# Performance work log

Measured on AMD Instinct MI355X. Metric: run time of the kernel, lower is better.

Reference implementation:

```python
import jax, jax.numpy as jnp
import numpy as np


def _gelu(x):
    # torch nn.GELU default is the exact (erf) variant
    return jax.nn.gelu(x, approximate=False)


def setup_inputs() -> dict:
    key = jax.random.key(0)
    ks = jax.random.split(key, 10)
    B, IN, H, D, C, K = 32768, 64, 256, 16, 8, 64
    HS = D // 2  # structure_filter hidden (latent_dim > 2)

    def rn(k, shape, scale):
        return jax.random.normal(k, shape, dtype=jnp.float32) * scale

    x = rn(ks[0], (B, IN), 1.0)
    W1 = rn(ks[1], (IN, H), 1.0 / np.sqrt(IN)); b1 = jnp.zeros((H,), jnp.float32)
    W2 = rn(ks[2], (H, H), 1.0 / np.sqrt(H));   b2 = jnp.zeros((H,), jnp.float32)
    Wv = rn(ks[3], (H, D), 1.0 / np.sqrt(H));   bv = jnp.zeros((D,), jnp.float32)
    chart_centers = rn(ks[4], (C, D), 0.02)
    codebook = rn(ks[5], (C, K, D), 0.02)
    sf_W1 = rn(ks[6], (D, HS), 1.0 / np.sqrt(D));  sf_b1 = jnp.zeros((HS,), jnp.float32)
    sf_W2 = rn(ks[7], (HS, D), 1.0 / np.sqrt(HS)); sf_b2 = jnp.zeros((D,), jnp.float32)
    return {
        "x": x, "W1": W1, "b1": b1, "W2": W2, "b2": b2, "Wv": Wv, "bv": bv,
        "chart_centers": chart_centers, "codebook": codebook,
        "sf_W1": sf_W1, "sf_b1": sf_b1, "sf_W2": sf_W2, "sf_b2": sf_b2,
    }


def reference(x, W1, b1, W2, b2, Wv, bv, chart_centers, codebook, sf_W1, sf_b1, sf_W2, sf_b2):
    sg = jax.lax.stop_gradient
    # feature extractor: Linear -> GELU -> Linear -> GELU
    f = _gelu(x @ W1 + b1)
    f = _gelu(f @ W2 + b2)
    v = f @ Wv + bv                                        # [B, D]
    D = v.shape[-1]
    C = codebook.shape[0]
    # chart routing
    scores = (v @ chart_centers.T) / jnp.sqrt(jnp.float32(D))   # [B, C]
    router_weights = jax.nn.softmax(scores, axis=-1)
    K_chart = jnp.argmax(router_weights, axis=1)                 # [B]
    c_bar = router_weights @ chart_centers                       # [B, D]
    v_local = v - c_bar
    # per-chart codebook distances
    diff = v_local[:, None, None, :] - codebook[None]            # [B, C, K, D]
    dist = jnp.sum(diff * diff, axis=-1)                         # [B, C, K]
    indices = jnp.argmin(dist, axis=-1)                          # [B, C]
    z_q_all = codebook[jnp.arange(C)[None, :], indices]          # [B, C, D]
    # VQ losses (router weights detached)
    w = sg(router_weights)[:, :, None]                           # [B, C, 1]
    v_bc = v_local[:, None, :]                                   # [B, 1, D]
    commitment = jnp.sum(jnp.mean((v_bc - sg(z_q_all)) ** 2 * w, axis=(0, 2)))
    codebook_loss = jnp.sum(jnp.mean((z_q_all - sg(v_bc)) ** 2 * w, axis=(0, 2)))
    vq_loss = codebook_loss + 0.25 * commitment
    z_q_blended = jnp.sum(z_q_all * router_weights[:, :, None], axis=1)   # [B, D]
    K_code = jnp.take_along_axis(indices, K_chart[:, None], axis=1)[:, 0]  # [B]
    # structure filter on per-chart residuals
    delta = v_bc - sg(z_q_all)                                   # [B, C, D]
    z_n_all_charts = _gelu(delta @ sf_W1 + sf_b1) @ sf_W2 + sf_b2  # [B, C, D]
    z_n = jnp.sum(z_n_all_charts * router_weights[:, :, None], axis=1)
    z_tex = (v_local - sg(z_q_blended)) - z_n
    z_q_st = v_local + sg(z_q_blended - v_local)                 # straight-through
    z_geo = c_bar + z_q_st + z_n
    return (K_chart, K_code, z_n, z_tex, router_weights, z_geo, vq_loss,
            indices, z_n_all_charts, c_bar)
```

## Files before the change

kernel.cpp:

```cpp
#include <hip/hip_runtime.h>
#include <hip/hip_bf16.h>

#define O0 0ull
#define O1 32768ull
#define O2 65536ull
#define O3 589824ull
#define O4 1114112ull
#define O5 1376256ull
#define O6 1900544ull
#define O7 1900545ull
#define O8 2162689ull
#define O9 6356993ull

static constexpr int    ENI  = 16;
static constexpr int    END  = 10;
static constexpr double EW   = 4.27 / 16.0;
static constexpr double EIW  = 16.0 / 4.27;

struct ErfTab { double a[ENI][END]; };

static constexpr double cexp_pos_(double x) {
    double s = 1.0, term = 1.0;
    for (int n = 1; n < 200; ++n) {
        term = term * x / (double)n;
        s += term;
        if (term < 1e-22 * s) break;
    }
    return s;
}
static constexpr ErfTab make_erftab_() {
    ErfTab T{};
    const double k2p = 1.12837916709551257390;
    double c0 = 0.5 * EW;
    double erf_cur = 0.0;
    {
        double u = c0 * c0, term = c0, s = 0.0;
        for (int n = 0; n < 40; ++n) { s += term / (double)(2 * n + 1); term *= -u / (double)(n + 1); }
        erf_cur = k2p * s;
    }
    const int NS = 24;
    for (int i = 0; i < ENI; ++i) {
        double c = ((double)i + 0.5) * EW;
        double e2 = k2p / cexp_pos_(c * c);
        double H[NS]; double a[NS + 1];
        H[0] = 1.0; H[1] = 2.0 * c;
        for (int n = 2; n < NS; ++n) H[n] = 2.0 * c * H[n - 1] - 2.0 * (double)(n - 1) * H[n - 2];
        a[0] = erf_cur;
        double fact = 1.0;
        for (int n = 1; n <= NS; ++n) {
            fact *= (double)n;
            double sgn = ((n - 1) & 1) ? -1.0 : 1.0;
            a[n] = sgn * H[n - 1] * e2 / fact;
        }
        for (int j = 0; j < END; ++j) T.a[i][j] = a[j];
        double s = 0.0, hp = 1.0;
        for (int n = 0; n <= NS; ++n) { s += a[n] * hp; hp *= EW; }
        erf_cur = s;
    }
    return T;
}
__constant__ ErfTab G_ERFTAB = make_erftab_();

__device__ __forceinline__ float erf_np_t(float t, const double* se) {
#pragma clang fp contract(off)
    double x = fabs((double)t);
    int idx = (int)(x * EIW);
    idx = idx > 15 ? 15 : idx;
    const double* A = se + idx * END;
    double d = x - ((double)idx + 0.5) * EW;
    double2 a89 = *(const double2*)(A + 8);
    double2 a67 = *(const double2*)(A + 6);
    double2 a45 = *(const double2*)(A + 4);
    double2 a23 = *(const double2*)(A + 2);
    double2 a01 = *(const double2*)(A + 0);
    double p = a89.y;
    p = fma(p, d, a89.x);
    p = fma(p, d, a67.y); p = fma(p, d, a67.x);
    p = fma(p, d, a45.y); p = fma(p, d, a45.x);
    p = fma(p, d, a23.y); p = fma(p, d, a23.x);
    p = fma(p, d, a01.y); p = fma(p, d, a01.x);
    float e = (x >= 4.1) ? 1.0f : (float)p;
    return (t < 0.0f) ? -e : e;
}

__device__ __forceinline__ float4 gelu4_np(float4 z, const double* se) {
#pragma clang fp contract(off)
    const float s2 = 0x1.6a09e6p+0f;
    float4 r;
    float e0 = erf_np_t(z.x / s2, se);
    float e1 = erf_np_t(z.y / s2, se);
    float e2 = erf_np_t(z.z / s2, se);
    float e3 = erf_np_t(z.w / s2, se);
    r.x = (z.x * (e0 + 1.0f)) / 2.0f;
    r.y = (z.y * (e1 + 1.0f)) / 2.0f;
    r.z = (z.z * (e2 + 1.0f)) / 2.0f;
    r.w = (z.w * (e3 + 1.0f)) / 2.0f;
    return r;
}

__global__ __launch_bounds__(256) void fused_mlp_np_k(
    const float* __restrict__ x,  const float* __restrict__ W1,
    const float* __restrict__ b1, const float* __restrict__ W2,
    const float* __restrict__ b2, const float* __restrict__ Wv,
    const float* __restrict__ bv, float* __restrict__ vout)
{
#pragma clang fp contract(off)
    __shared__ float  ft[32][260];
    __shared__ double serf[ENI * END];
    const int t  = threadIdx.x;
    const int w  = t >> 6;
    const int cg = t & 63;
    const int r0 = blockIdx.x * 32;
    const int rb = w * 8;

    if (t < ENI * END) serf[t] = ((const double*)&G_ERFTAB)[t];
    __syncthreads();

    float acc[8][4];
#pragma unroll
    for (int i = 0; i < 8; ++i) { acc[i][0]=0.f; acc[i][1]=0.f; acc[i][2]=0.f; acc[i][3]=0.f; }

    for (int k0 = 0; k0 < 64; k0 += 4) {
        float4 w0 = *(const float4*)(W1 + (size_t)(k0 + 0) * 256 + cg * 4);
        float4 w1 = *(const float4*)(W1 + (size_t)(k0 + 1) * 256 + cg * 4);
        float4 w2 = *(const float4*)(W1 + (size_t)(k0 + 2) * 256 + cg * 4);
        float4 w3 = *(const float4*)(W1 + (size_t)(k0 + 3) * 256 + cg * 4);
#pragma unroll
        for (int rr = 0; rr < 8; ++rr) {
            float4 a = *(const float4*)(x + (size_t)(r0 + rb + rr) * 64 + k0);
            acc[rr][0] = fmaf(a.x, w0.x, acc[rr][0]);
            acc[rr][1] = fmaf(a.x, w0.y, acc[rr][1]);
            acc[rr][2] = fmaf(a.x, w0.z, acc[rr][2]);
            acc[rr][3] = fmaf(a.x, w0.w, acc[rr][3]);
            acc[rr][0] = fmaf(a.y, w1.x, acc[rr][0]);
            acc[rr][1] = fmaf(a.y, w1.y, acc[rr][1]);
            acc[rr][2] = fmaf(a.y, w1.z, acc[rr][2]);
            acc[rr][3] = fmaf(a.y, w1.w, acc[rr][3]);
            acc[rr][0] = fmaf(a.z, w2.x, acc[rr][0]);
            acc[rr][1] = fmaf(a.z, w2.y, acc[rr][1]);
            acc[rr][2] = fmaf(a.z, w2.z, acc[rr][2]);
            acc[rr][3] = fmaf(a.z, w2.w, acc[rr][3]);
            acc[rr][0] = fmaf(a.w, w3.x, acc[rr][0]);
            acc[rr][1] = fmaf(a.w, w3.y, acc[rr][1]);
            acc[rr][2] = fmaf(a.w, w3.z, acc[rr][2]);
            acc[rr][3] = fmaf(a.w, w3.w, acc[rr][3]);
        }
    }
    {
        float4 bb = *(const float4*)(b1 + cg * 4);
#pragma unroll
        for (int rr = 0; rr < 8; ++rr) {
            float4 z = make_float4(acc[rr][0] + bb.x, acc[rr][1] + bb.y,
                                   acc[rr][2] + bb.z, acc[rr][3] + bb.w);
            *(float4*)&ft[rb + rr][cg * 4] = gelu4_np(z, serf);
        }
    }

#pragma unroll
    for (int i = 0; i < 8; ++i) { acc[i][0]=0.f; acc[i][1]=0.f; acc[i][2]=0.f; acc[i][3]=0.f; }
    for (int k0 = 0; k0 < 256; k0 += 4) {
        float4 w0 = *(const float4*)(W2 + (size_t)(k0 + 0) * 256 + cg * 4);
        float4 w1 = *(const float4*)(W2 + (size_t)(k0 + 1) * 256 + cg * 4);
        float4 w2 = *(const float4*)(W2 + (size_t)(k0 + 2) * 256 + cg * 4);
        float4 w3 = *(const float4*)(W2 + (size_t)(k0 + 3) * 256 + cg * 4);
#pragma unroll
        for (int rr = 0; rr < 8; ++rr) {
            float4 a = *(const float4*)&ft[rb + rr][k0];
            acc[rr][0] = fmaf(a.x, w0.x, acc[rr][0]);
            acc[rr][1] = fmaf(a.x, w0.y, acc[rr][1]);
            acc[rr][2] = fmaf(a.x, w0.z, acc[rr][2]);
            acc[rr][3] = fmaf(a.x, w0.w, acc[rr][3]);
            acc[rr][0] = fmaf(a.y, w1.x, acc[rr][0]);
            acc[rr][1] = fmaf(a.y, w1.y, acc[rr][1]);
            acc[rr][2] = fmaf(a.y, w1.z, acc[rr][2]);
            acc[rr][3] = fmaf(a.y, w1.w, acc[rr][3]);
            acc[rr][0] = fmaf(a.z, w2.x, acc[rr][0]);
            acc[rr][1] = fmaf(a.z, w2.y, acc[rr][1]);
            acc[rr][2] = fmaf(a.z, w2.z, acc[rr][2]);
            acc[rr][3] = fmaf(a.z, w2.w, acc[rr][3]);
            acc[rr][0] = fmaf(a.w, w3.x, acc[rr][0]);
            acc[rr][1] = fmaf(a.w, w3.y, acc[rr][1]);
            acc[rr][2] = fmaf(a.w, w3.z, acc[rr][2]);
            acc[rr][3] = fmaf(a.w, w3.w, acc[rr][3]);
        }
    }
    {
        float4 bb = *(const float4*)(b2 + cg * 4);
#pragma unroll
        for (int rr = 0; rr < 8; ++rr) {
            float4 z = make_float4(acc[rr][0] + bb.x, acc[rr][1] + bb.y,
                                   acc[rr][2] + bb.z, acc[rr][3] + bb.w);
            *(float4*)&ft[rb + rr][cg * 4] = gelu4_np(z, serf);
        }
    }
    __syncthreads();

    {
        const int vrow = t & 31;
        const int d0   = (t >> 5) * 2;
        float a0 = 0.f, a1 = 0.f;
        for (int k4 = 0; k4 < 256; k4 += 4) {
            float4 f = *(const float4*)&ft[vrow][k4];
            float2 q0 = *(const float2*)(Wv + (size_t)(k4 + 0) * 16 + d0);
            float2 q1 = *(const float2*)(Wv + (size_t)(k4 + 1) * 16 + d0);
            float2 q2 = *(const float2*)(Wv + (size_t)(k4 + 2) * 16 + d0);
            float2 q3 = *(const float2*)(Wv + (size_t)(k4 + 3) * 16 + d0);
            a0 = fmaf(f.x, q0.x, a0);  a1 = fmaf(f.x, q0.y, a1);
            a0 = fmaf(f.y, q1.x, a0);  a1 = fmaf(f.y, q1.y, a1);
            a0 = fmaf(f.z, q2.x, a0);  a1 = fmaf(f.z, q2.y, a1);
            a0 = fmaf(f.w, q3.x, a0);  a1 = fmaf(f.w, q3.y, a1);
        }
        float2 o = make_float2(a0 + bv[d0], a1 + bv[d0 + 1]);
        *(float2*)&vout[(size_t)(r0 + vrow) * 16 + d0] = o;
    }
}

__global__ __launch_bounds__(256) void atlas_np_k(
    const float* __restrict__ vbuf, const float* __restrict__ cc,
    const float* __restrict__ cb,   const float* __restrict__ sfW1,
    const float* __restrict__ sfb1, const float* __restrict__ sfW2,
    const float* __restrict__ sfb2, float* __restrict__ out,
    float* __restrict__ partials)
{
#pragma clang fp contract(off)
    __shared__ float scb[8448];
    __shared__ float scc[128];
    __shared__ float sW1[128];
    __shared__ float sW2[128];
    __shared__ float sb1[8];
    __shared__ float sb2[16];
    __shared__ float red[4];
    __shared__ double serf[ENI * END];

    const int t = threadIdx.x;
    for (int i = t; i < 8192; i += 256) {
        int c = i >> 10, rem = i & 1023, kk = rem >> 4, d = rem & 15;
        scb[c * 1032 + kk * 16 + d] = cb[i];
    }
    if (t < 128) { scc[t] = cc[t]; sW1[t] = sfW1[t]; sW2[t] = sfW2[t]; }
    if (t < 8)  sb1[t] = sfb1[t];
    if (t < 16) sb2[t] = sfb2[t];
    if (t >= 64 && t < 64 + ENI * END) serf[t - 64] = ((const double*)&G_ERFTAB)[t - 64];
    __syncthreads();

    const int c    = t & 7;
    const int rloc = t >> 3;
    const int lane = t & 63;
    const int lb   = lane & ~7;
    const int row  = blockIdx.x * 32 + rloc;

    float v[16];
    {
        const float4* vp = (const float4*)(vbuf + (size_t)row * 16);
        float4 a = vp[0], b = vp[1], g = vp[2], h4 = vp[3];
        v[0]=a.x;  v[1]=a.y;  v[2]=a.z;  v[3]=a.w;
        v[4]=b.x;  v[5]=b.y;  v[6]=b.z;  v[7]=b.w;
        v[8]=g.x;  v[9]=g.y;  v[10]=g.z; v[11]=g.w;
        v[12]=h4.x; v[13]=h4.y; v[14]=h4.z; v[15]=h4.w;
    }

    float score = 0.f;
#pragma unroll
    for (int d = 0; d < 16; ++d) score = fmaf(v[d], scc[c * 16 + d], score);
    score = score / 4.0f;

    float m = score;
#pragma unroll
    for (int off = 1; off < 8; off <<= 1) m = fmaxf(m, __shfl_xor(m, off));
    float e = (float)exp((double)(score - m));
    float ea[8];
#pragma unroll
    for (int j = 0; j < 8; ++j) ea[j] = __shfl(e, lb + j);
    float s = ((ea[0] + ea[1]) + (ea[2] + ea[3])) + ((ea[4] + ea[5]) + (ea[6] + ea[7]));
    float rw = e / s;

    float rwa[8];
#pragma unroll
    for (int j = 0; j < 8; ++j) rwa[j] = ea[j] / s;

    float bmv = rwa[0]; int bci = 0;
#pragma unroll
    for (int j = 1; j < 8; ++j) if (rwa[j] > bmv) { bmv = rwa[j]; bci = j; }

    float cbar[16], vl[16];
#pragma unroll
    for (int d = 0; d < 16; ++d) {
        float a = 0.f;
#pragma unroll
        for (int j = 0; j < 8; ++j) a = fmaf(rwa[j], scc[j * 16 + d], a);
        cbar[d] = a;
        vl[d]   = v[d] - a;
    }

    const float* cbc = scb + c * 1032;
    float bd = 3.4e38f; int bk = 0; bool first = true;
    for (int kk = 0; kk < 64; ++kk) {
        const float4* q = (const float4*)(cbc + kk * 16);
        float4 q0 = q[0], q1 = q[1], q2 = q[2], q3 = q[3];
        float sq[16];
        float dd;
        dd = vl[0]  - q0.x; sq[0]  = dd * dd;
        dd = vl[1]  - q0.y; sq[1]  = dd * dd;
        dd = vl[2]  - q0.z; sq[2]  = dd * dd;
        dd = vl[3]  - q0.w; sq[3]  = dd * dd;
        dd = vl[4]  - q1.x; sq[4]  = dd * dd;
        dd = vl[5]  - q1.y; sq[5]  = dd * dd;
        dd = vl[6]  - q1.z; sq[6]  = dd * dd;
        dd = vl[7]  - q1.w; sq[7]  = dd * dd;
        dd = vl[8]  - q2.x; sq[8]  = dd * dd;
        dd = vl[9]  - q2.y; sq[9]  = dd * dd;
        dd = vl[10] - q2.z; sq[10] = dd * dd;
        dd = vl[11] - q2.w; sq[11] = dd * dd;
        dd = vl[12] - q3.x; sq[12] = dd * dd;
        dd = vl[13] - q3.y; sq[13] = dd * dd;
        dd = vl[14] - q3.z; sq[14] = dd * dd;
        dd = vl[15] - q3.w; sq[15] = dd * dd;
        float r0_ = sq[0] + sq[8],  r1_ = sq[1] + sq[9];
        float r2_ = sq[2] + sq[10], r3_ = sq[3] + sq[11];
        float r4_ = sq[4] + sq[12], r5_ = sq[5] + sq[13];
        float r6_ = sq[6] + sq[14], r7_ = sq[7] + sq[15];
        float dist = ((r0_ + r1_) + (r2_ + r3_)) + ((r4_ + r5_) + (r6_ + r7_));
        if (first || dist < bd) { bd = dist; bk = kk; first = false; }
    }

    float zq[16];
    {
        const float4* q = (const float4*)(cbc + bk * 16);
        float4 q0 = q[0], q1 = q[1], q2 = q[2], q3 = q[3];
        zq[0]=q0.x;  zq[1]=q0.y;  zq[2]=q0.z;  zq[3]=q0.w;
        zq[4]=q1.x;  zq[5]=q1.y;  zq[6]=q1.z;  zq[7]=q1.w;
        zq[8]=q2.x;  zq[9]=q2.y;  zq[10]=q2.z; zq[11]=q2.w;
        zq[12]=q3.x; zq[13]=q3.y; zq[14]=q3.z; zq[15]=q3.w;
    }

    float del[16];
#pragma unroll
    for (int d = 0; d < 16; ++d) del[d] = vl[d] - zq[d];

    float pa[8];
#pragma unroll
    for (int j = 0; j < 8; ++j) {
        float a = 0.f;
#pragma unroll
        for (int d = 0; d < 16; ++d) a = fmaf(del[d], sW1[d * 8 + j], a);
        pa[j] = a + sb1[j];
    }
    float4 g0 = gelu4_np(make_float4(pa[0], pa[1], pa[2], pa[3]), serf);
    float4 g1 = gelu4_np(make_float4(pa[4], pa[5], pa[6], pa[7]), serf);
    float h[8] = { g0.x, g0.y, g0.z, g0.w, g1.x, g1.y, g1.z, g1.w };

    float zn[16];
#pragma unroll
    for (int d = 0; d < 16; ++d) {
        float a = 0.f;
#pragma unroll
        for (int j = 0; j < 8; ++j) a = fmaf(h[j], sW2[j * 16 + d], a);
        zn[d] = a + sb2[d];
    }

    float ls = 0.f;
#pragma unroll
    for (int d = 0; d < 16; ++d) ls = fmaf(del[d], del[d], ls);
    ls *= rw;

    __syncthreads();
    float* zql = scb;
    float* znl = scb + 4224;
    {
        float* pq = zql + rloc * 132 + c * 16;
        float* pn = znl + rloc * 132 + c * 16;
        *(float4*)&pq[0]  = make_float4(zq[0],  zq[1],  zq[2],  zq[3]);
        *(float4*)&pq[4]  = make_float4(zq[4],  zq[5],  zq[6],  zq[7]);
        *(float4*)&pq[8]  = make_float4(zq[8],  zq[9],  zq[10], zq[11]);
        *(float4*)&pq[12] = make_float4(zq[12], zq[13], zq[14], zq[15]);
        *(float4*)&pn[0]  = make_float4(zn[0],  zn[1],  zn[2],  zn[3]);
        *(float4*)&pn[4]  = make_float4(zn[4],  zn[5],  zn[6],  zn[7]);
        *(float4*)&pn[8]  = make_float4(zn[8],  zn[9],  zn[10], zn[11]);
        *(float4*)&pn[12] = make_float4(zn[12], zn[13], zn[14], zn[15]);
    }
    __syncthreads();

    const int dd0 = c * 2;
    float aq0 = 0.f, aq1 = 0.f, an0 = 0.f, an1 = 0.f;
#pragma unroll
    for (int j = 0; j < 8; ++j) {
        float2 qv = *(const float2*)&zql[rloc * 132 + j * 16 + dd0];
        float2 nv = *(const float2*)&znl[rloc * 132 + j * 16 + dd0];
        float p0 = qv.x * rwa[j]; aq0 = aq0 + p0;
        float p1 = qv.y * rwa[j]; aq1 = aq1 + p1;
        float p2 = nv.x * rwa[j]; an0 = an0 + p2;
        float p3 = nv.y * rwa[j]; an1 = an1 + p3;
    }

    out[O4 + (size_t)row * 8 + c] = rw;
    out[O7 + (size_t)row * 8 + c] = (float)bk;
    {
        float* p = out + O8 + (size_t)row * 128 + c * 16;
#pragma unroll
        for (int d = 0; d < 16; ++d) p[d] = zn[d];
    }
    if (c == 0)   out[O0 + row] = (float)bci;
    if (c == bci) out[O1 + row] = (float)bk;
    {
        int d = dd0;
        float zst0 = vl[d]     + (aq0 - vl[d]);
        float zst1 = vl[d + 1] + (aq1 - vl[d + 1]);
        out[O2 + (size_t)row * 16 + d]     = an0;
        out[O2 + (size_t)row * 16 + d + 1] = an1;
        out[O3 + (size_t)row * 16 + d]     = (vl[d]     - aq0) - an0;
        out[O3 + (size_t)row * 16 + d + 1] = (vl[d + 1] - aq1) - an1;
        out[O5 + (size_t)row * 16 + d]     = (cbar[d]     + zst0) + an0;
        out[O5 + (size_t)row * 16 + d + 1] = (cbar[d + 1] + zst1) + an1;
        out[O9 + (size_t)row * 16 + d]     = cbar[d];
        out[O9 + (size_t)row * 16 + d + 1] = cbar[d + 1];
    }

#pragma unroll
    for (int off = 1; off < 64; off <<= 1) ls += __shfl_xor(ls, off);
    if ((t & 63) == 0) red[t >> 6] = ls;
    __syncthreads();
    if (t == 0) partials[blockIdx.x] = red[0] + red[1] + red[2] + red[3];
}

__global__ __launch_bounds__(256) void loss_reduce_k(
    const float* __restrict__ partials, float* __restrict__ out)
{
    __shared__ float sm[256];
    const int t = threadIdx.x;
    float a = 0.f;
    for (int i = t; i < 1024; i += 256) a += partials[i];
    sm[t] = a;
    __syncthreads();
    for (int s2 = 128; s2 > 0; s2 >>= 1) {
        if (t < s2) sm[t] += sm[t + s2];
        __syncthreads();
    }
    if (t == 0) out[O6] = sm[0] * (1.25f / 524288.0f);
}

extern "C" void kernel_launch(void* const* d_in, const int* in_sizes, int n_in,
                              void* d_out, int out_size, void* d_ws, size_t ws_size,
                              hipStream_t stream) {
    (void)in_sizes; (void)n_in; (void)out_size;
    const float* x    = (const float*)d_in[0];
    const float* W1   = (const float*)d_in[1];
    const float* b1   = (const float*)d_in[2];
    const float* W2   = (const float*)d_in[3];
    const float* b2   = (const float*)d_in[4];
    const float* Wv   = (const float*)d_in[5];
    const float* bv   = (const float*)d_in[6];
    const float* cc   = (const float*)d_in[7];
    const float* cb   = (const float*)d_in[8];
    const float* sfW1 = (const float*)d_in[9];
    const float* sfb1 = (const float*)d_in[10];
    const float* sfW2 = (const float*)d_in[11];
    const float* sfb2 = (const float*)d_in[12];
    float* out = (float*)d_out;

    float* vbuf = (float*)d_ws;
    float* partials = vbuf + (size_t)32768 * 16;
    if (ws_size < ((size_t)32768 * 16 + 1024) * 4) return;

    fused_mlp_np_k<<<1024, 256, 0, stream>>>(x, W1, b1, W2, b2, Wv, bv, vbuf);
    atlas_np_k    <<<1024, 256, 0, stream>>>(vbuf, cc, cb, sfW1, sfb1, sfW2, sfb2, out, partials);
    loss_reduce_k <<<1, 256, 0, stream>>>(partials, out);
}
```

Measured before the change: 155.8 us.

## Stage W2 into LDS with double-buffered async global-to-LDS loads

The second MLP layer no longer has each wavefront read W2 rows straight from global memory. W2 is now streamed in 8-row chunks into a double-buffered shared-memory area with the global_load_lds builtin, so the next chunk is fetched while the current one is consumed. This aims to cut redundant global/L1 traffic, since all four waves of a block read the same W2 rows, and to hide load latency. In exchange it adds 32 block-wide barriers per block and about 16 KB more LDS, which may lower occupancy. Correctness also relies on the barrier waiting for the async LDS writes to finish.

```diff
diff --git a/kernel.cpp b/kernel.cpp
--- a/kernel.cpp
+++ b/kernel.cpp
@@ -98,6 +98,12 @@
     return r;
 }
 
+__device__ __forceinline__ void gl_lds16(const float* g, float* l) {
+    __builtin_amdgcn_global_load_lds(
+        (const __attribute__((address_space(1))) void*)g,
+        (__attribute__((address_space(3))) void*)l, 16, 0, 0);
+}
+
 __global__ __launch_bounds__(256) void fused_mlp_np_k(
     const float* __restrict__ x,  const float* __restrict__ W1,
     const float* __restrict__ b1, const float* __restrict__ W2,
@@ -106,15 +112,28 @@
 {
 #pragma clang fp contract(off)
     __shared__ float  ft[32][260];
+    __shared__ float  wbuf[2][2048];
     __shared__ double serf[ENI * END];
     const int t  = threadIdx.x;
     const int w  = t >> 6;
     const int cg = t & 63;
+    const int l  = t & 63;
     const int r0 = blockIdx.x * 32;
     const int rb = w * 8;
 
     if (t < ENI * END) serf[t] = ((const double*)&G_ERFTAB)[t];
     __syncthreads();
+
+    auto issueW2 = [&](int c, int b) {
+        const int seg = w * 2;
+#pragma unroll
+        for (int j = 0; j < 2; ++j) {
+            const float* src = W2 + (size_t)c * 2048 + (size_t)(seg + j) * 256 + l * 4;
+            gl_lds16(src, &wbuf[b][(seg + j) * 256]);
+        }
+    };
+
+    issueW2(0, 0);
 
     float acc[8][4];
 #pragma unroll
@@ -158,30 +177,37 @@
 
 #pragma unroll
     for (int i = 0; i < 8; ++i) { acc[i][0]=0.f; acc[i][1]=0.f; acc[i][2]=0.f; acc[i][3]=0.f; }
-    for (int k0 = 0; k0 < 256; k0 += 4) {
-        float4 w0 = *(const float4*)(W2 + (size_t)(k0 + 0) * 256 + cg * 4);
-        float4 w1 = *(const float4*)(W2 + (size_t)(k0 + 1) * 256 + cg * 4);
-        float4 w2 = *(const float4*)(W2 + (size_t)(k0 + 2) * 256 + cg * 4);
-        float4 w3 = *(const float4*)(W2 + (size_t)(k0 + 3) * 256 + cg * 4);
-#pragma unroll
-        for (int rr = 0; rr < 8; ++rr) {
-            float4 a = *(const float4*)&ft[rb + rr][k0];
-            acc[rr][0] = fmaf(a.x, w0.x, acc[rr][0]);
-            acc[rr][1] = fmaf(a.x, w0.y, acc[rr][1]);
-            acc[rr][2] = fmaf(a.x, w0.z, acc[rr][2]);
-            acc[rr][3] = fmaf(a.x, w0.w, acc[rr][3]);
-            acc[rr][0] = fmaf(a.y, w1.x, acc[rr][0]);
-            acc[rr][1] = fmaf(a.y, w1.y, acc[rr][1]);
-            acc[rr][2] = fmaf(a.y, w1.z, acc[rr][2]);
-            acc[rr][3] = fmaf(a.y, w1.w, acc[rr][3]);
-            acc[rr][0] = fmaf(a.z, w2.x, acc[rr][0]);
-            acc[rr][1] = fmaf(a.z, w2.y, acc[rr][1]);
-            acc[rr][2] = fmaf(a.z, w2.z, acc[rr][2]);
-            acc[rr][3] = fmaf(a.z, w2.w, acc[rr][3]);
-            acc[rr][0] = fmaf(a.w, w3.x, acc[rr][0]);
-            acc[rr][1] = fmaf(a.w, w3.y, acc[rr][1]);
-            acc[rr][2] = fmaf(a.w, w3.z, acc[rr][2]);
-            acc[rr][3] = fmaf(a.w, w3.w, acc[rr][3]);
+
+    for (int c = 0; c < 32; ++c) {
+        __syncthreads();
+        if (c < 31) issueW2(c + 1, (c + 1) & 1);
+        const int b = c & 1;
+#pragma unroll
+        for (int kk = 0; kk < 8; kk += 4) {
+            float4 w0 = *(const float4*)&wbuf[b][(kk + 0) * 256 + cg * 4];
+            float4 w1 = *(const float4*)&wbuf[b][(kk + 1) * 256 + cg * 4];
+            float4 w2 = *(const float4*)&wbuf[b][(kk + 2) * 256 + cg * 4];
+            float4 w3 = *(const float4*)&wbuf[b][(kk + 3) * 256 + cg * 4];
+#pragma unroll
+            for (int rr = 0; rr < 8; ++rr) {
+                float4 a = *(const float4*)&ft[rb + rr][c * 8 + kk];
+                acc[rr][0] = fmaf(a.x, w0.x, acc[rr][0]);
+                acc[rr][1] = fmaf(a.x, w0.y, acc[rr][1]);
+                acc[rr][2] = fmaf(a.x, w0.z, acc[rr][2]);
+                acc[rr][3] = fmaf(a.x, w0.w, acc[rr][3]);
+                acc[rr][0] = fmaf(a.y, w1.x, acc[rr][0]);
+                acc[rr][1] = fmaf(a.y, w1.y, acc[rr][1]);
+                acc[rr][2] = fmaf(a.y, w1.z, acc[rr][2]);
+                acc[rr][3] = fmaf(a.y, w1.w, acc[rr][3]);
+                acc[rr][0] = fmaf(a.z, w2.x, acc[rr][0]);
+                acc[rr][1] = fmaf(a.z, w2.y, acc[rr][1]);
+                acc[rr][2] = fmaf(a.z, w2.z, acc[rr][2]);
+                acc[rr][3] = fmaf(a.z, w2.w, acc[rr][3]);
+                acc[rr][0] = fmaf(a.w, w3.x, acc[rr][0]);
+                acc[rr][1] = fmaf(a.w, w3.y, acc[rr][1]);
+                acc[rr][2] = fmaf(a.w, w3.z, acc[rr][2]);
+                acc[rr][3] = fmaf(a.w, w3.w, acc[rr][3]);
+            }
         }
     }
     {
```

Result: slower. 162.4 us (+4.2%).

## Fuse MLP and atlas kernels into one kernel sharing an LDS buffer

Applied to the files above, without the earlier changes.

Merges the feature-extractor MLP kernel and the chart/codebook atlas kernel into a single kernel. The per-row v vector now stays in shared memory instead of going through a global workspace, and one shared buffer is reused for the MLP activations, the codebook copy and the z_q/z_n staging. This removes one kernel launch and the global write and read of v. In exchange, each block now also loads the codebook after the MLP with an extra barrier, and the LDS padding strides change.

```diff
diff --git a/kernel.cpp b/kernel.cpp
--- a/kernel.cpp
+++ b/kernel.cpp
@@ -98,15 +98,27 @@
     return r;
 }
 
-__global__ __launch_bounds__(256) void fused_mlp_np_k(
+__global__ __launch_bounds__(256) void fused_all_k(
     const float* __restrict__ x,  const float* __restrict__ W1,
     const float* __restrict__ b1, const float* __restrict__ W2,
     const float* __restrict__ b2, const float* __restrict__ Wv,
-    const float* __restrict__ bv, float* __restrict__ vout)
+    const float* __restrict__ bv, const float* __restrict__ cc,
+    const float* __restrict__ cb, const float* __restrict__ sfW1,
+    const float* __restrict__ sfb1, const float* __restrict__ sfW2,
+    const float* __restrict__ sfb2, float* __restrict__ out,
+    float* __restrict__ partials)
 {
 #pragma clang fp contract(off)
-    __shared__ float  ft[32][260];
+    __shared__ float  ubuf[8320];
+    __shared__ float  sv[32][20];
     __shared__ double serf[ENI * END];
+    __shared__ float  scc[128];
+    __shared__ float  sW1[128];
+    __shared__ float  sW2[128];
+    __shared__ float  sb1[8];
+    __shared__ float  sb2[16];
+    __shared__ float  red[4];
+
     const int t  = threadIdx.x;
     const int w  = t >> 6;
     const int cg = t & 63;
@@ -114,7 +126,12 @@
     const int rb = w * 8;
 
     if (t < ENI * END) serf[t] = ((const double*)&G_ERFTAB)[t];
-    __syncthreads();
+    if (t < 128) { scc[t] = cc[t]; sW1[t] = sfW1[t]; sW2[t] = sfW2[t]; }
+    if (t >= 128 && t < 136) sb1[t - 128] = sfb1[t - 128];
+    if (t >= 136 && t < 152) sb2[t - 136] = sfb2[t - 136];
+    __syncthreads();
+
+    float* ft = ubuf;
 
     float acc[8][4];
 #pragma unroll
@@ -152,7 +169,7 @@
         for (int rr = 0; rr < 8; ++rr) {
             float4 z = make_float4(acc[rr][0] + bb.x, acc[rr][1] + bb.y,
                                    acc[rr][2] + bb.z, acc[rr][3] + bb.w);
-            *(float4*)&ft[rb + rr][cg * 4] = gelu4_np(z, serf);
+            *(float4*)&ft[(rb + rr) * 260 + cg * 4] = gelu4_np(z, serf);
         }
     }
 
@@ -165,7 +182,7 @@
         float4 w3 = *(const float4*)(W2 + (size_t)(k0 + 3) * 256 + cg * 4);
 #pragma unroll
         for (int rr = 0; rr < 8; ++rr) {
-            float4 a = *(const float4*)&ft[rb + rr][k0];
+            float4 a = *(const float4*)&ft[(rb + rr) * 260 + k0];
             acc[rr][0] = fmaf(a.x, w0.x, acc[rr][0]);
             acc[rr][1] = fmaf(a.x, w0.y, acc[rr][1]);
             acc[rr][2] = fmaf(a.x, w0.z, acc[rr][2]);
@@ -190,7 +207,7 @@
         for (int rr = 0; rr < 8; ++rr) {
             float4 z = make_float4(acc[rr][0] + bb.x, acc[rr][1] + bb.y,
                                    acc[rr][2] + bb.z, acc[rr][3] + bb.w);
-            *(float4*)&ft[rb + rr][cg * 4] = gelu4_np(z, serf);
+            *(float4*)&ft[(rb + rr) * 260 + cg * 4] = gelu4_np(z, serf);
         }
     }
     __syncthreads();
@@ -200,7 +217,7 @@
         const int d0   = (t >> 5) * 2;
         float a0 = 0.f, a1 = 0.f;
         for (int k4 = 0; k4 < 256; k4 += 4) {
-            float4 f = *(const float4*)&ft[vrow][k4];
+            float4 f = *(const float4*)&ft[vrow * 260 + k4];
             float2 q0 = *(const float2*)(Wv + (size_t)(k4 + 0) * 16 + d0);
             float2 q1 = *(const float2*)(Wv + (size_t)(k4 + 1) * 16 + d0);
             float2 q2 = *(const float2*)(Wv + (size_t)(k4 + 2) * 16 + d0);
@@ -210,49 +227,28 @@
             a0 = fmaf(f.z, q2.x, a0);  a1 = fmaf(f.z, q2.y, a1);
             a0 = fmaf(f.w, q3.x, a0);  a1 = fmaf(f.w, q3.y, a1);
         }
-        float2 o = make_float2(a0 + bv[d0], a1 + bv[d0 + 1]);
-        *(float2*)&vout[(size_t)(r0 + vrow) * 16 + d0] = o;
-    }
-}
-
-__global__ __launch_bounds__(256) void atlas_np_k(
-    const float* __restrict__ vbuf, const float* __restrict__ cc,
-    const float* __restrict__ cb,   const float* __restrict__ sfW1,
-    const float* __restrict__ sfb1, const float* __restrict__ sfW2,
-    const float* __restrict__ sfb2, float* __restrict__ out,
-    float* __restrict__ partials)
-{
-#pragma clang fp contract(off)
-    __shared__ float scb[8448];
-    __shared__ float scc[128];
-    __shared__ float sW1[128];
-    __shared__ float sW2[128];
-    __shared__ float sb1[8];
-    __shared__ float sb2[16];
-    __shared__ float red[4];
-    __shared__ double serf[ENI * END];
-
-    const int t = threadIdx.x;
+        *(float2*)&sv[vrow][d0] = make_float2(a0 + bv[d0], a1 + bv[d0 + 1]);
+    }
+    __syncthreads();
+
     for (int i = t; i < 8192; i += 256) {
         int c = i >> 10, rem = i & 1023, kk = rem >> 4, d = rem & 15;
-        scb[c * 1032 + kk * 16 + d] = cb[i];
-    }
-    if (t < 128) { scc[t] = cc[t]; sW1[t] = sfW1[t]; sW2[t] = sfW2[t]; }
-    if (t < 8)  sb1[t] = sfb1[t];
-    if (t < 16) sb2[t] = sfb2[t];
-    if (t >= 64 && t < 64 + ENI * END) serf[t - 64] = ((const double*)&G_ERFTAB)[t - 64];
+        ubuf[c * 1028 + kk * 16 + d] = cb[i];
+    }
     __syncthreads();
 
     const int c    = t & 7;
     const int rloc = t >> 3;
     const int lane = t & 63;
     const int lb   = lane & ~7;
-    const int row  = blockIdx.x * 32 + rloc;
+    const int row  = r0 + rloc;
 
     float v[16];
     {
-        const float4* vp = (const float4*)(vbuf + (size_t)row * 16);
-        float4 a = vp[0], b = vp[1], g = vp[2], h4 = vp[3];
+        float4 a = *(const float4*)&sv[rloc][0];
+        float4 b = *(const float4*)&sv[rloc][4];
+        float4 g = *(const float4*)&sv[rloc][8];
+        float4 h4 = *(const float4*)&sv[rloc][12];
         v[0]=a.x;  v[1]=a.y;  v[2]=a.z;  v[3]=a.w;
         v[4]=b.x;  v[5]=b.y;  v[6]=b.z;  v[7]=b.w;
         v[8]=g.x;  v[9]=g.y;  v[10]=g.z; v[11]=g.w;
@@ -292,7 +288,7 @@
         vl[d]   = v[d] - a;
     }
 
-    const float* cbc = scb + c * 1032;
+    const float* cbc = ubuf + c * 1028;
     float bd = 3.4e38f; int bk = 0; bool first = true;
     for (int kk = 0; kk < 64; ++kk) {
         const float4* q = (const float4*)(cbc + kk * 16);
@@ -364,11 +360,11 @@
     ls *= rw;
 
     __syncthreads();
-    float* zql = scb;
-    float* znl = scb + 4224;
-    {
-        float* pq = zql + rloc * 132 + c * 16;
-        float* pn = znl + rloc * 132 + c * 16;
+    float* zql = ubuf;
+    float* znl = ubuf + 4160;
+    {
+        float* pq = zql + rloc * 130 + c * 16;
+        float* pn = znl + rloc * 130 + c * 16;
         *(float4*)&pq[0]  = make_float4(zq[0],  zq[1],  zq[2],  zq[3]);
         *(float4*)&pq[4]  = make_float4(zq[4],  zq[5],  zq[6],  zq[7]);
         *(float4*)&pq[8]  = make_float4(zq[8],  zq[9],  zq[10], zq[11]);
@@ -384,8 +380,8 @@
     float aq0 = 0.f, aq1 = 0.f, an0 = 0.f, an1 = 0.f;
 #pragma unroll
     for (int j = 0; j < 8; ++j) {
-        float2 qv = *(const float2*)&zql[rloc * 132 + j * 16 + dd0];
-        float2 nv = *(const float2*)&znl[rloc * 132 + j * 16 + dd0];
+        float2 qv = *(const float2*)&zql[rloc * 130 + j * 16 + dd0];
+        float2 nv = *(const float2*)&znl[rloc * 130 + j * 16 + dd0];
         float p0 = qv.x * rwa[j]; aq0 = aq0 + p0;
         float p1 = qv.y * rwa[j]; aq1 = aq1 + p1;
         float p2 = nv.x * rwa[j]; an0 = an0 + p2;
@@ -457,11 +453,11 @@
     const float* sfb2 = (const float*)d_in[12];
     float* out = (float*)d_out;
 
-    float* vbuf = (float*)d_ws;
-    float* partials = vbuf + (size_t)32768 * 16;
-    if (ws_size < ((size_t)32768 * 16 + 1024) * 4) return;
-
-    fused_mlp_np_k<<<1024, 256, 0, stream>>>(x, W1, b1, W2, b2, Wv, bv, vbuf);
-    atlas_np_k    <<<1024, 256, 0, stream>>>(vbuf, cc, cb, sfW1, sfb1, sfW2, sfb2, out, partials);
-    loss_reduce_k <<<1, 256, 0, stream>>>(partials, out);
-}
+    float* partials = (float*)d_ws;
+    if (ws_size < 1024 * 4) return;
+
+    fused_all_k<<<1024, 256, 0, stream>>>(x, W1, b1, W2, b2, Wv, bv,
+                                          cc, cb, sfW1, sfb1, sfW2, sfb2,
+                                          out, partials);
+    loss_reduce_k<<<1, 256, 0, stream>>>(partials, out);
+}
```

New measurement: 156.1 us. Within noise of the previous version (+0.2%).
